# Kernel tuning notes

Hardware: AMD Instinct MI355X
Metric: run time of the kernel (lower is better)

## Reference

```python
import jax, jax.numpy as jnp
import numpy as np

NEG_SLOPE = 0.01  # F.leaky_relu default
EPS = 1e-6


def setup_inputs() -> dict:
    key = jax.random.key(0)
    k1, k2, k3, k4 = jax.random.split(key, 4)
    N, E, IN, OUT = 100000, 1600000, 128, 64
    x = jax.random.normal(k1, (N, IN), dtype=jnp.float32)
    W = jax.random.normal(k2, (OUT, IN), dtype=jnp.float32) * (1.0 / np.sqrt(IN))
    a = jax.random.uniform(k3, (2 * OUT,), dtype=jnp.float32)  # uniform [0,1) as in init
    edge_index = jax.random.randint(k4, (2, E), 0, N, dtype=jnp.int64)
    return {"x": x, "W": W, "a": a, "edge_index": edge_index}


def reference(x, W, a, edge_index):
    N = x.shape[0]
    out_f = W.shape[0]
    # add self loops: append (i, i) for every node
    loops = jnp.arange(N, dtype=edge_index.dtype)
    ei = jnp.concatenate([edge_index, jnp.stack([loops, loops])], axis=1)
    src, dst = ei[0], ei[1]

    messages = x @ W.T                      # [N, out]
    h_src = messages[src]                   # [E', out]
    h_dst = messages[dst]                   # [E', out]

    # e = cat([h_dst, h_src]) . a  == h_dst.a[:out] + h_src.a[out:]
    e = h_dst @ a[:out_f] + h_src @ a[out_f:]
    e = jnp.where(e >= 0, e, NEG_SLOPE * e)  # leaky_relu
    w = jnp.exp(e)                           # unnormalized edge weights

    denom = jax.ops.segment_sum(w, dst, num_segments=N)                     # [N]
    agg = jax.ops.segment_sum(h_src * w[:, None], dst, num_segments=N)      # [N, out]
    return agg / jnp.clip(denom, EPS)[:, None]
```

## Files before the change

kernel.cpp:

```cpp
#include <hip/hip_runtime.h>
#include <hip/hip_bf16.h>

#define IN_F 128
#define OUT_F 64
#define NEG 0.01f

#define BUCKET_N 256
#define EPB 8192
#define CAP 48
#define MAXB 512
#define MAXSLAB 512
#define CMAXIT 32

__device__ __forceinline__ float leaky_exp(float e) {
    e = (e >= 0.f) ? e : NEG * e;
    return expf(e);
}

__device__ __forceinline__ float b2f(unsigned int v) { return __uint_as_float(v); }

__global__ __launch_bounds__(512) void gemm_msg_kernel(
    const float* __restrict__ x, const float* __restrict__ W,
    const float* __restrict__ a,
    __hip_bfloat16* __restrict__ msg, float2* __restrict__ ab, int N)
{
    __shared__ float Wt[IN_F * 64];
    const int tid = threadIdx.x;
    const int base = blockIdx.x * 128;

#pragma unroll
    for (int t = 0; t < 4; ++t) {
        int i = tid + t * 512;
        int o = i & 63;
        int k4 = i >> 6;
        float4 wv = ((const float4*)W)[o * (IN_F / 4) + k4];
        Wt[(k4 * 4 + 0) * 64 + o] = wv.x;
        Wt[(k4 * 4 + 1) * 64 + o] = wv.y;
        Wt[(k4 * 4 + 2) * 64 + o] = wv.z;
        Wt[(k4 * 4 + 3) * 64 + o] = wv.w;
    }
    __syncthreads();

    const int tx = tid & 15;
    const int ty = tid >> 4;

    const float4* xr[4];
#pragma unroll
    for (int ri = 0; ri < 4; ++ri) {
        int row = min(base + ty * 4 + ri, N - 1);
        xr[ri] = (const float4*)x + (size_t)row * (IN_F / 4);
    }

    float4 xc[4];
#pragma unroll
    for (int ri = 0; ri < 4; ++ri) xc[ri] = xr[ri][0];

    float acc[4][4] = {};
#pragma unroll 2
    for (int k4 = 0; k4 < IN_F / 4; ++k4) {
        float4 xn[4];
        const int kn = min(k4 + 1, IN_F / 4 - 1);
#pragma unroll
        for (int ri = 0; ri < 4; ++ri) xn[ri] = xr[ri][kn];

        float wq[4][4];
#pragma unroll
        for (int j = 0; j < 4; ++j)
            *(float4*)wq[j] = *(const float4*)&Wt[(k4 * 4 + j) * 64 + tx * 4];
        float xq[4][4];
#pragma unroll
        for (int ri = 0; ri < 4; ++ri) *(float4*)xq[ri] = xc[ri];

#pragma unroll
        for (int ri = 0; ri < 4; ++ri)
#pragma unroll
            for (int ci = 0; ci < 4; ++ci) {
                acc[ri][ci] += xq[ri][0] * wq[0][ci];
                acc[ri][ci] += xq[ri][1] * wq[1][ci];
                acc[ri][ci] += xq[ri][2] * wq[2][ci];
                acc[ri][ci] += xq[ri][3] * wq[3][ci];
            }
#pragma unroll
        for (int ri = 0; ri < 4; ++ri) xc[ri] = xn[ri];
    }

    float a_lo[4], a_hi[4];
#pragma unroll
    for (int ci = 0; ci < 4; ++ci) {
        a_lo[ci] = a[tx * 4 + ci];
        a_hi[ci] = a[OUT_F + tx * 4 + ci];
    }

#pragma unroll
    for (int ri = 0; ri < 4; ++ri) {
        int row = base + ty * 4 + ri;
        if (row < N) {
            union { ushort4 u; __hip_bfloat16 h[4]; } pk;
            pk.h[0] = __float2bfloat16(acc[ri][0]);
            pk.h[1] = __float2bfloat16(acc[ri][1]);
            pk.h[2] = __float2bfloat16(acc[ri][2]);
            pk.h[3] = __float2bfloat16(acc[ri][3]);
            *(ushort4*)&msg[(size_t)row * OUT_F + tx * 4] = pk.u;
        }
        float pa = acc[ri][0] * a_lo[0] + acc[ri][1] * a_lo[1] +
                   acc[ri][2] * a_lo[2] + acc[ri][3] * a_lo[3];
        float pb = acc[ri][0] * a_hi[0] + acc[ri][1] * a_hi[1] +
                   acc[ri][2] * a_hi[2] + acc[ri][3] * a_hi[3];
#pragma unroll
        for (int off = 1; off < 16; off <<= 1) {
            pa += __shfl_xor(pa, off);
            pb += __shfl_xor(pb, off);
        }
        if (tx == 0 && row < N) ab[row] = make_float2(pa, pb);
    }
}

__global__ __launch_bounds__(512) void partition_kernel(
    const int* __restrict__ src, const int* __restrict__ dst,
    int* __restrict__ counts, unsigned int* __restrict__ cells,
    int* __restrict__ bucket_tot, int E, int B, int NBLKP)
{
    __shared__ int cnt_s[MAXB];
    for (int i = threadIdx.x; i < B; i += 512) cnt_s[i] = 0;
    __syncthreads();

    const size_t pbase = (size_t)blockIdx.x * B;

#pragma unroll
    for (int u = 0; u < 4; ++u) {
        const int i4 = blockIdx.x * 2048 + u * 512 + threadIdx.x;
        const int e0 = i4 * 4;
        if (e0 + 3 < E) {
            int4 s4 = ((const int4*)src)[i4];
            int4 d4 = ((const int4*)dst)[i4];
            int b0 = d4.x >> 8, b1 = d4.y >> 8, b2 = d4.z >> 8, b3 = d4.w >> 8;
            int r0 = atomicAdd(&cnt_s[b0], 1);
            int r1 = atomicAdd(&cnt_s[b1], 1);
            int r2 = atomicAdd(&cnt_s[b2], 1);
            int r3 = atomicAdd(&cnt_s[b3], 1);
            if (r0 < CAP) cells[(pbase + b0) * CAP + r0] =
                (unsigned)s4.x | ((unsigned)(d4.x & 255) << 20);
            if (r1 < CAP) cells[(pbase + b1) * CAP + r1] =
                (unsigned)s4.y | ((unsigned)(d4.y & 255) << 20);
            if (r2 < CAP) cells[(pbase + b2) * CAP + r2] =
                (unsigned)s4.z | ((unsigned)(d4.z & 255) << 20);
            if (r3 < CAP) cells[(pbase + b3) * CAP + r3] =
                (unsigned)s4.w | ((unsigned)(d4.w & 255) << 20);
        } else {
            for (int e = e0; e < E && e < e0 + 4; ++e) {
                int s = src[e], d = dst[e];
                int b = d >> 8;
                int r = atomicAdd(&cnt_s[b], 1);
                if (r < CAP) cells[(pbase + b) * CAP + r] =
                    (unsigned)s | ((unsigned)(d & 255) << 20);
            }
        }
    }
    __syncthreads();
    for (int i = threadIdx.x; i < B; i += 512) {
        int c = min(cnt_s[i], CAP);
        counts[(size_t)i * NBLKP + blockIdx.x] = c;
        atomicAdd(&bucket_tot[i], c);
    }
}

__global__ __launch_bounds__(512) void bucket_scan_kernel(
    const int* __restrict__ bucket_tot, int* __restrict__ bucket_base,
    int* __restrict__ offs, int N, int B)
{
    __shared__ int tmp[512];
    const int t = threadIdx.x;
    int v = 0;
    if (t < B) {
        int nodes = N - t * BUCKET_N;
        nodes = max(0, min(BUCKET_N, nodes));
        v = bucket_tot[t] + nodes;
    }
    tmp[t] = v;
    __syncthreads();
#pragma unroll
    for (int d = 1; d < 512; d <<= 1) {
        int add = (t >= d) ? tmp[t - d] : 0;
        __syncthreads();
        tmp[t] += add;
        __syncthreads();
    }
    if (t < B) bucket_base[t] = tmp[t] - v;
    if (t == 511) offs[N] = tmp[511];
}

__global__ __launch_bounds__(512) void compact_kernel(
    const int* __restrict__ counts, const unsigned int* __restrict__ cells,
    const int* __restrict__ bucket_base, const float2* __restrict__ ab,
    int* __restrict__ offs, int2* __restrict__ edges,
    int N, int B, int NBLK, int NBLKP)
{
    __shared__ int cnt_l[MAXSLAB];
    __shared__ int hist[BUCKET_N];
    __shared__ int scan_s[BUCKET_N];
    __shared__ int cursor[BUCKET_N];
    __shared__ float alpha_s[BUCKET_N];
    const int b = blockIdx.x;
    const int tid = threadIdx.x;
    const int wave = tid >> 6, lane = tid & 63;

    for (int i = tid; i < NBLK; i += 512) cnt_l[i] = counts[(size_t)b * NBLKP + i];
    float2 myab = make_float2(0.f, 0.f);
    if (tid < BUCKET_N) {
        int g = b * BUCKET_N + tid;
        bool valid = (g < N);
        hist[tid] = valid ? 1 : 0;
        if (valid) myab = ab[g];
        alpha_s[tid] = myab.x;
    }
    __syncthreads();

    unsigned cell_c[CMAXIT];
#pragma unroll
    for (int it = 0; it < CMAXIT; ++it) {
        int sl = wave + it * 8;
        unsigned v = 0xFFFFFFFFu;
        if (sl < NBLK) {
            int c = cnt_l[sl];
            if (lane < c) {
                v = cells[((size_t)sl * B + b) * CAP + lane];
                atomicAdd(&hist[v >> 20], 1);
            }
        }
        cell_c[it] = v;
    }
    for (int sl = wave + CMAXIT * 8; sl < NBLK; sl += 8) {
        int c = cnt_l[sl];
        if (lane < c) {
            unsigned v = cells[((size_t)sl * B + b) * CAP + lane];
            atomicAdd(&hist[v >> 20], 1);
        }
    }
    __syncthreads();

    int hv = 0;
    if (tid < BUCKET_N) { hv = hist[tid]; scan_s[tid] = hv; }
    __syncthreads();
#pragma unroll
    for (int d = 1; d < BUCKET_N; d <<= 1) {
        int add = (tid < BUCKET_N && tid >= d) ? scan_s[tid - d] : 0;
        __syncthreads();
        if (tid < BUCKET_N) scan_s[tid] += add;
        __syncthreads();
    }
    const int gbase = bucket_base[b];
    if (tid < BUCKET_N) {
        int excl = scan_s[tid] - hv;
        int g = b * BUCKET_N + tid;
        if (g < N) {
            offs[g] = gbase + excl;
            float wself = leaky_exp(myab.x + myab.y);
            edges[gbase + excl] = make_int2(g, __float_as_int(wself));
            cursor[tid] = excl + 1;
        }
    }
    __syncthreads();

#pragma unroll
    for (int it = 0; it < CMAXIT; ++it) {
        unsigned v = cell_c[it];
        if (v != 0xFFFFFFFFu) {
            int s = v & 0xFFFFF;
            int l = (v >> 20) & 255;
            float w = leaky_exp(alpha_s[l] + ab[s].y);
            int pos = atomicAdd(&cursor[l], 1);
            edges[gbase + pos] = make_int2(s, __float_as_int(w));
        }
    }
    for (int sl = wave + CMAXIT * 8; sl < NBLK; sl += 8) {
        int c = cnt_l[sl];
        if (lane < c) {
            unsigned v = cells[((size_t)sl * B + b) * CAP + lane];
            int s = v & 0xFFFFF;
            int l = (v >> 20) & 255;
            float w = leaky_exp(alpha_s[l] + ab[s].y);
            int pos = atomicAdd(&cursor[l], 1);
            edges[gbase + pos] = make_int2(s, __float_as_int(w));
        }
    }
}

__global__ __launch_bounds__(256) void aggregate_kernel(
    const int* __restrict__ offs, const int2* __restrict__ edges,
    const __hip_bfloat16* __restrict__ msg,
    float* __restrict__ out, int N)
{
    const int tid = threadIdx.x;
    const int node = blockIdx.x * 8 + (tid >> 5);
    if (node >= N) return;
    const int half = tid & 31;
    const int g = half & 7;
    const int u = half >> 3;

    const unsigned int* msp32 = (const unsigned int*)msg;

    float acc[8] = {0.f, 0.f, 0.f, 0.f, 0.f, 0.f, 0.f, 0.f};
    float den = 0.f;

    const int st = offs[node], en = offs[node + 1];
    const int deg = en - st;

    int idx = st + u;
    int j = 0;
    for (; j + 16 <= deg; j += 16) {
#pragma unroll
        for (int q = 0; q < 4; ++q) {
            int2 e = edges[idx + q * 4];
            float w = __int_as_float(e.y);
            uint4 m = *(const uint4*)&msp32[(size_t)e.x * (OUT_F / 2) + 4 * g];
            acc[0] += w * b2f(m.x << 16);
            acc[1] += w * b2f(m.x & 0xFFFF0000u);
            acc[2] += w * b2f(m.y << 16);
            acc[3] += w * b2f(m.y & 0xFFFF0000u);
            acc[4] += w * b2f(m.z << 16);
            acc[5] += w * b2f(m.z & 0xFFFF0000u);
            acc[6] += w * b2f(m.w << 16);
            acc[7] += w * b2f(m.w & 0xFFFF0000u);
            den += w;
        }
        idx += 16;
    }
    for (; j < deg; j += 4) {
        int ii = min(idx, en - 1);
        int2 e = edges[ii];
        float w = (idx < en) ? __int_as_float(e.y) : 0.f;
        uint4 m = *(const uint4*)&msp32[(size_t)e.x * (OUT_F / 2) + 4 * g];
        acc[0] += w * b2f(m.x << 16);
        acc[1] += w * b2f(m.x & 0xFFFF0000u);
        acc[2] += w * b2f(m.y << 16);
        acc[3] += w * b2f(m.y & 0xFFFF0000u);
        acc[4] += w * b2f(m.z << 16);
        acc[5] += w * b2f(m.z & 0xFFFF0000u);
        acc[6] += w * b2f(m.w << 16);
        acc[7] += w * b2f(m.w & 0xFFFF0000u);
        den += w;
        idx += 4;
    }

#pragma unroll
    for (int off = 8; off <= 16; off <<= 1) {
#pragma unroll
        for (int i = 0; i < 8; ++i) acc[i] += __shfl_xor(acc[i], off);
        den += __shfl_xor(den, off);
    }

    if (u == 0) {
        float dn = 1.f / fmaxf(den, 1e-6f);
        float4* op = (float4*)&out[(size_t)node * OUT_F + 8 * g];
        op[0] = make_float4(acc[0] * dn, acc[1] * dn, acc[2] * dn, acc[3] * dn);
        op[1] = make_float4(acc[4] * dn, acc[5] * dn, acc[6] * dn, acc[7] * dn);
    }
}

extern "C" void kernel_launch(void* const* d_in, const int* in_sizes, int n_in,
                              void* d_out, int out_size, void* d_ws, size_t ws_size,
                              hipStream_t stream) {
    const float* x  = (const float*)d_in[0];
    const float* W  = (const float*)d_in[1];
    const float* a  = (const float*)d_in[2];
    const int*   ei = (const int*)d_in[3];
    float* out = (float*)d_out;

    const int IN = in_sizes[1] / OUT_F;
    const int N  = in_sizes[0] / IN;
    const int E  = in_sizes[3] / 2;
    const int B  = (N + BUCKET_N - 1) / BUCKET_N;
    const int NBLK  = (E + EPB - 1) / EPB;
    const int NBLKP = (NBLK + 3) & ~3;

    auto align16 = [](size_t v) { return (v + 15) & ~(size_t)15; };
    char* p = (char*)d_ws;
    __hip_bfloat16* msg = (__hip_bfloat16*)p; p += align16((size_t)N * OUT_F * 2);
    float2* ab    = (float2*)p; p += align16((size_t)N * 8);
    int*   counts = (int*)p;   p += align16((size_t)B * NBLKP * 4);
    unsigned int* cells = (unsigned int*)p; p += align16((size_t)NBLK * B * CAP * 4);
    int*   btot   = (int*)p;   p += align16((size_t)B * 4);
    int*   bbase  = (int*)p;   p += align16((size_t)B * 4);
    int*   offs   = (int*)p;   p += align16((size_t)(N + 1) * 4);
    int2*  edges  = (int2*)p;  p += align16((size_t)(E + N) * 8);

    const int* esrc = ei;
    const int* edst = ei + E;

    hipMemsetAsync(btot, 0, (size_t)B * 4, stream);

    gemm_msg_kernel<<<(N + 127) / 128, 512, 0, stream>>>(x, W, a, msg, ab, N);
    partition_kernel<<<NBLK, 512, 0, stream>>>(esrc, edst, counts, cells,
                                               btot, E, B, NBLKP);
    bucket_scan_kernel<<<1, 512, 0, stream>>>(btot, bbase, offs, N, B);
    compact_kernel<<<B, 512, 0, stream>>>(counts, cells, bbase, ab,
                                          offs, edges, N, B, NBLK, NBLKP);
    aggregate_kernel<<<(N + 7) / 8, 256, 0, stream>>>(offs, edges, msg, out, N);
}
```

Baseline: 135.5 us.

## Quantize messages to int16 and aggregate with integer weights after per-node max subtraction

Messages are stored as fixed-point int16 (scale 128) instead of bf16. Compact now stores the leaky logits rather than exp weights. Aggregation first finds each node's max logit, then builds 15-bit integer weights with exp2 and accumulates them with 24-bit integer multiplies. CAP is also raised from 48 to 64. The aim is cheaper integer accumulation, at the cost of an extra pass over the edge list, coarser precision, possible int16 overflow if messages exceed ±256, and more cell storage.

```diff
diff --git a/kernel.cpp b/kernel.cpp
--- a/kernel.cpp
+++ b/kernel.cpp
@@ -4,25 +4,25 @@
 #define IN_F 128
 #define OUT_F 64
 #define NEG 0.01f
+#define LOG2E 1.4426950408889634f
+#define WSBITS 15.0f
+#define MSGSCALE 128.0f
 
 #define BUCKET_N 256
 #define EPB 8192
-#define CAP 48
+#define CAP 64
 #define MAXB 512
 #define MAXSLAB 512
 #define CMAXIT 32
 
-__device__ __forceinline__ float leaky_exp(float e) {
-    e = (e >= 0.f) ? e : NEG * e;
-    return expf(e);
-}
-
-__device__ __forceinline__ float b2f(unsigned int v) { return __uint_as_float(v); }
+__device__ __forceinline__ float leaky(float e) {
+    return (e >= 0.f) ? e : NEG * e;
+}
 
 __global__ __launch_bounds__(512) void gemm_msg_kernel(
     const float* __restrict__ x, const float* __restrict__ W,
     const float* __restrict__ a,
-    __hip_bfloat16* __restrict__ msg, float2* __restrict__ ab, int N)
+    short* __restrict__ msgq, float2* __restrict__ ab, int N)
 {
     __shared__ float Wt[IN_F * 64];
     const int tid = threadIdx.x;
@@ -95,12 +95,12 @@
     for (int ri = 0; ri < 4; ++ri) {
         int row = base + ty * 4 + ri;
         if (row < N) {
-            union { ushort4 u; __hip_bfloat16 h[4]; } pk;
-            pk.h[0] = __float2bfloat16(acc[ri][0]);
-            pk.h[1] = __float2bfloat16(acc[ri][1]);
-            pk.h[2] = __float2bfloat16(acc[ri][2]);
-            pk.h[3] = __float2bfloat16(acc[ri][3]);
-            *(ushort4*)&msg[(size_t)row * OUT_F + tx * 4] = pk.u;
+            short4 q;
+            q.x = (short)__float2int_rn(acc[ri][0] * MSGSCALE);
+            q.y = (short)__float2int_rn(acc[ri][1] * MSGSCALE);
+            q.z = (short)__float2int_rn(acc[ri][2] * MSGSCALE);
+            q.w = (short)__float2int_rn(acc[ri][3] * MSGSCALE);
+            *(short4*)&msgq[(size_t)row * OUT_F + tx * 4] = q;
         }
         float pa = acc[ri][0] * a_lo[0] + acc[ri][1] * a_lo[1] +
                    acc[ri][2] * a_lo[2] + acc[ri][3] * a_lo[3];
@@ -254,8 +254,8 @@
         int g = b * BUCKET_N + tid;
         if (g < N) {
             offs[g] = gbase + excl;
-            float wself = leaky_exp(myab.x + myab.y);
-            edges[gbase + excl] = make_int2(g, __float_as_int(wself));
+            float lg = leaky(myab.x + myab.y);
+            edges[gbase + excl] = make_int2(g, __float_as_int(lg));
             cursor[tid] = excl + 1;
         }
     }
@@ -267,9 +267,9 @@
         if (v != 0xFFFFFFFFu) {
             int s = v & 0xFFFFF;
             int l = (v >> 20) & 255;
-            float w = leaky_exp(alpha_s[l] + ab[s].y);
+            float lg = leaky(alpha_s[l] + ab[s].y);
             int pos = atomicAdd(&cursor[l], 1);
-            edges[gbase + pos] = make_int2(s, __float_as_int(w));
+            edges[gbase + pos] = make_int2(s, __float_as_int(lg));
         }
     }
     for (int sl = wave + CMAXIT * 8; sl < NBLK; sl += 8) {
@@ -278,16 +278,16 @@
             unsigned v = cells[((size_t)sl * B + b) * CAP + lane];
             int s = v & 0xFFFFF;
             int l = (v >> 20) & 255;
-            float w = leaky_exp(alpha_s[l] + ab[s].y);
+            float lg = leaky(alpha_s[l] + ab[s].y);
             int pos = atomicAdd(&cursor[l], 1);
-            edges[gbase + pos] = make_int2(s, __float_as_int(w));
+            edges[gbase + pos] = make_int2(s, __float_as_int(lg));
         }
     }
 }
 
 __global__ __launch_bounds__(256) void aggregate_kernel(
     const int* __restrict__ offs, const int2* __restrict__ edges,
-    const __hip_bfloat16* __restrict__ msg,
+    const short* __restrict__ msgq,
     float* __restrict__ out, int N)
 {
     const int tid = threadIdx.x;
@@ -297,13 +297,19 @@
     const int g = half & 7;
     const int u = half >> 3;
 
-    const unsigned int* msp32 = (const unsigned int*)msg;
-
-    float acc[8] = {0.f, 0.f, 0.f, 0.f, 0.f, 0.f, 0.f, 0.f};
-    float den = 0.f;
+    const unsigned int* msp32 = (const unsigned int*)msgq;
 
     const int st = offs[node], en = offs[node + 1];
     const int deg = en - st;
+
+    float m = -3.0e38f;
+    for (int ii = st + u; ii < en; ii += 4)
+        m = fmaxf(m, __int_as_float(edges[ii].y));
+    m = fmaxf(m, __shfl_xor(m, 8));
+    m = fmaxf(m, __shfl_xor(m, 16));
+
+    int iacc[8] = {0, 0, 0, 0, 0, 0, 0, 0};
+    int iden = 0;
 
     int idx = st + u;
     int j = 0;
@@ -311,49 +317,52 @@
 #pragma unroll
         for (int q = 0; q < 4; ++q) {
             int2 e = edges[idx + q * 4];
-            float w = __int_as_float(e.y);
-            uint4 m = *(const uint4*)&msp32[(size_t)e.x * (OUT_F / 2) + 4 * g];
-            acc[0] += w * b2f(m.x << 16);
-            acc[1] += w * b2f(m.x & 0xFFFF0000u);
-            acc[2] += w * b2f(m.y << 16);
-            acc[3] += w * b2f(m.y & 0xFFFF0000u);
-            acc[4] += w * b2f(m.z << 16);
-            acc[5] += w * b2f(m.z & 0xFFFF0000u);
-            acc[6] += w * b2f(m.w << 16);
-            acc[7] += w * b2f(m.w & 0xFFFF0000u);
-            den += w;
+            int wsi = (int)exp2f(fmaf(__int_as_float(e.y) - m, LOG2E, WSBITS));
+            uint4 mv = *(const uint4*)&msp32[(size_t)e.x * (OUT_F / 2) + 4 * g];
+            iacc[0] += __mul24(wsi, (int)(short)(mv.x & 0xFFFFu));
+            iacc[1] += __mul24(wsi, ((int)mv.x) >> 16);
+            iacc[2] += __mul24(wsi, (int)(short)(mv.y & 0xFFFFu));
+            iacc[3] += __mul24(wsi, ((int)mv.y) >> 16);
+            iacc[4] += __mul24(wsi, (int)(short)(mv.z & 0xFFFFu));
+            iacc[5] += __mul24(wsi, ((int)mv.z) >> 16);
+            iacc[6] += __mul24(wsi, (int)(short)(mv.w & 0xFFFFu));
+            iacc[7] += __mul24(wsi, ((int)mv.w) >> 16);
+            iden += wsi;
         }
         idx += 16;
     }
     for (; j < deg; j += 4) {
         int ii = min(idx, en - 1);
         int2 e = edges[ii];
-        float w = (idx < en) ? __int_as_float(e.y) : 0.f;
-        uint4 m = *(const uint4*)&msp32[(size_t)e.x * (OUT_F / 2) + 4 * g];
-        acc[0] += w * b2f(m.x << 16);
-        acc[1] += w * b2f(m.x & 0xFFFF0000u);
-        acc[2] += w * b2f(m.y << 16);
-        acc[3] += w * b2f(m.y & 0xFFFF0000u);
-        acc[4] += w * b2f(m.z << 16);
-        acc[5] += w * b2f(m.z & 0xFFFF0000u);
-        acc[6] += w * b2f(m.w << 16);
-        acc[7] += w * b2f(m.w & 0xFFFF0000u);
-        den += w;
+        int wsi = (idx < en)
+            ? (int)exp2f(fmaf(__int_as_float(e.y) - m, LOG2E, WSBITS)) : 0;
+        uint4 mv = *(const uint4*)&msp32[(size_t)e.x * (OUT_F / 2) + 4 * g];
+        iacc[0] += __mul24(wsi, (int)(short)(mv.x & 0xFFFFu));
+        iacc[1] += __mul24(wsi, ((int)mv.x) >> 16);
+        iacc[2] += __mul24(wsi, (int)(short)(mv.y & 0xFFFFu));
+        iacc[3] += __mul24(wsi, ((int)mv.y) >> 16);
+        iacc[4] += __mul24(wsi, (int)(short)(mv.z & 0xFFFFu));
+        iacc[5] += __mul24(wsi, ((int)mv.z) >> 16);
+        iacc[6] += __mul24(wsi, (int)(short)(mv.w & 0xFFFFu));
+        iacc[7] += __mul24(wsi, ((int)mv.w) >> 16);
+        iden += wsi;
         idx += 4;
     }
 
 #pragma unroll
     for (int off = 8; off <= 16; off <<= 1) {
 #pragma unroll
-        for (int i = 0; i < 8; ++i) acc[i] += __shfl_xor(acc[i], off);
-        den += __shfl_xor(den, off);
+        for (int i = 0; i < 8; ++i) iacc[i] += __shfl_xor(iacc[i], off);
+        iden += __shfl_xor(iden, off);
     }
 
     if (u == 0) {
-        float dn = 1.f / fmaxf(den, 1e-6f);
+        float dn = 1.f / ((float)iden * MSGSCALE);
         float4* op = (float4*)&out[(size_t)node * OUT_F + 8 * g];
-        op[0] = make_float4(acc[0] * dn, acc[1] * dn, acc[2] * dn, acc[3] * dn);
-        op[1] = make_float4(acc[4] * dn, acc[5] * dn, acc[6] * dn, acc[7] * dn);
+        op[0] = make_float4((float)iacc[0] * dn, (float)iacc[1] * dn,
+                            (float)iacc[2] * dn, (float)iacc[3] * dn);
+        op[1] = make_float4((float)iacc[4] * dn, (float)iacc[5] * dn,
+                            (float)iacc[6] * dn, (float)iacc[7] * dn);
     }
 }
 
@@ -375,7 +384,7 @@
 
     auto align16 = [](size_t v) { return (v + 15) & ~(size_t)15; };
     char* p = (char*)d_ws;
-    __hip_bfloat16* msg = (__hip_bfloat16*)p; p += align16((size_t)N * OUT_F * 2);
+    short* msgq   = (short*)p; p += align16((size_t)N * OUT_F * 2);
     float2* ab    = (float2*)p; p += align16((size_t)N * 8);
     int*   counts = (int*)p;   p += align16((size_t)B * NBLKP * 4);
     unsigned int* cells = (unsigned int*)p; p += align16((size_t)NBLK * B * CAP * 4);
@@ -389,11 +398,11 @@
 
     hipMemsetAsync(btot, 0, (size_t)B * 4, stream);
 
-    gemm_msg_kernel<<<(N + 127) / 128, 512, 0, stream>>>(x, W, a, msg, ab, N);
+    gemm_msg_kernel<<<(N + 127) / 128, 512, 0, stream>>>(x, W, a, msgq, ab, N);
     partition_kernel<<<NBLK, 512, 0, stream>>>(esrc, edst, counts, cells,
                                                btot, E, B, NBLKP);
     bucket_scan_kernel<<<1, 512, 0, stream>>>(btot, bbase, offs, N, B);
     compact_kernel<<<B, 512, 0, stream>>>(counts, cells, bbase, ab,
                                           offs, edges, N, B, NBLK, NBLKP);
-    aggregate_kernel<<<(N + 7) / 8, 256, 0, stream>>>(offs, edges, msg, out, N);
-}
+    aggregate_kernel<<<(N + 7) / 8, 256, 0, stream>>>(offs, edges, msgq, out, N);
+}
```

Measured after the change: 142.1 us. +4.9%, slower.
